# Kernel optimization log

Measured on AMD Instinct MI355X. Metric: run time of the kernel, lower is better.

Reference implementation:

```python
import jax, jax.numpy as jnp
import numpy as np

GRID_SIZE = 5


def kan_layer(x, spline_weight, spline_scaler, grid):
    # x: (B, In); spline_weight: (Out, In, G); spline_scaler: (Out, In); grid: (G,)
    xn = jnp.tanh(x)                                   # (B, In)
    # distances: (B, Out, In, G) via broadcast of (B,1,In,1) against (G,)
    distances = jnp.abs(xn[:, None, :, None] - grid)
    weights = jnp.exp(-distances * spline_scaler[None, :, :, None])
    # double sum over grid then in_features, fused into one einsum
    return jnp.einsum('boig,oig->bo', weights, spline_weight)


def setup_inputs() -> dict:
    key = jax.random.key(0)
    ks = jax.random.split(key, 7)
    B, D_IN, D_H, D_OUT = 2048, 128, 256, 64
    return {
        'x':  jax.random.normal(ks[0], (B, D_IN), dtype=jnp.float32),
        'w1': jax.random.normal(ks[1], (D_H, D_IN, GRID_SIZE), dtype=jnp.float32),
        's1': jax.random.normal(ks[2], (D_H, D_IN), dtype=jnp.float32),
        'w2': jax.random.normal(ks[3], (D_H // 2, D_H, GRID_SIZE), dtype=jnp.float32),
        's2': jax.random.normal(ks[4], (D_H // 2, D_H), dtype=jnp.float32),
        'w3': jax.random.normal(ks[5], (D_OUT, D_H // 2, GRID_SIZE), dtype=jnp.float32),
        's3': jax.random.normal(ks[6], (D_OUT, D_H // 2), dtype=jnp.float32),
    }


def reference(x, w1, s1, w2, s2, w3, s3):
    grid = jnp.linspace(-1.0, 1.0, GRID_SIZE, dtype=jnp.float32)  # registered buffer
    h1 = jax.nn.relu(kan_layer(x, w1, s1, grid))
    h2 = jax.nn.relu(kan_layer(h1, w2, s2, grid))
    out = jax.nn.sigmoid(kan_layer(h2, w3, s3, grid))
    return out
```

## Files before the change

kernel.cpp:

```cpp
#include <hip/hip_runtime.h>
#include <math.h>

#define GRID_N 5
#define LOG2E 1.4426950408889634f
#define EXP2F __builtin_amdgcn_exp2f

__device__ __forceinline__ void prep_one(const float* __restrict__ w,
                                         const float* __restrict__ s,
                                         float* __restrict__ T, float* __restrict__ Kt,
                                         int O, int I, int idx) {
    int o = idx / I, i = idx % I;
    float K = -s[idx] * LOG2E;
    const float gv[5] = {-1.f, -0.5f, 0.f, 0.5f, 1.f};
    float A[6], B[6];
    A[0] = 0.f; B[5] = 0.f;
#pragma unroll
    for (int g = 0; g < 5; g++)
        A[g + 1] = A[g] + w[idx * GRID_N + g] * EXP2F(-K * gv[g]);
#pragma unroll
    for (int g = 4; g >= 0; g--)
        B[g] = B[g + 1] + w[idx * GRID_N + g] * EXP2F(K * gv[g]);
#pragma unroll
    for (int k = 0; k < 6; k++) {
        T[((i * 6 + k) * O + o) * 2 + 0] = A[k];
        T[((i * 6 + k) * O + o) * 2 + 1] = B[k];
    }
    Kt[i * O + o] = K;
}

__global__ __launch_bounds__(256) void prep_all(
    const float* __restrict__ w1, const float* __restrict__ s1, float* T1, float* K1,
    const float* __restrict__ w2, const float* __restrict__ s2, float* T2, float* K2,
    const float* __restrict__ w3, const float* __restrict__ s3, float* T3, float* K3) {
    int idx = blockIdx.x * 256 + threadIdx.x;
    if (idx < 32768)       prep_one(w1, s1, T1, K1, 256, 128, idx);
    else if (idx < 65536)  prep_one(w2, s2, T2, K2, 128, 256, idx - 32768);
    else if (idx < 73728)  prep_one(w3, s3, T3, K3,  64, 128, idx - 65536);
}

template<int IN, int OUT, int ACT, int BPT>
__global__ __launch_bounds__(256, 4) void kan_layer(
    const float* __restrict__ xin,
    const char*  __restrict__ Tb,
    const float* __restrict__ Kt,
    float* __restrict__ out)
{
    constexpr int CH  = IN / 64;
    constexpr int NBG = 2048 / BPT;
    constexpr unsigned ROWB = OUT * 8;

    const int lane = threadIdx.x & 63;
    const int wid  = (blockIdx.x << 2) | (threadIdx.x >> 6);
    const int oc   = wid / NBG;
    const int bg   = wid % NBG;
    const int o    = (oc << 6) | lane;
    const int b0   = bg * BPT;

    float    xv[BPT][CH];
    unsigned off[BPT][CH];
#pragma unroll
    for (int j = 0; j < BPT; j++)
#pragma unroll
        for (int c = 0; c < CH; c++) {
            int   i  = (c << 6) + lane;
            float v  = xin[(b0 + j) * IN + i];
            float ex = EXP2F(2.0f * LOG2E * v);
            float t  = 1.0f - 2.0f / (ex + 1.0f);
            xv[j][c] = t;
            int k = (int)((t + 1.0f) * 2.0f) + 1;
            k = k > 5 ? 5 : k;
            off[j][c] = (unsigned)(i * 6 + k) * ROWB;
        }

    float acc[BPT];
#pragma unroll
    for (int j = 0; j < BPT; j++) acc[j] = 0.f;

    const unsigned o8 = (unsigned)o * 8u;
    const float*   Kp = Kt + o;

#pragma unroll
    for (int c = 0; c < CH; c++) {
        for (int lb = 0; lb < 8; lb++) {
            float2 ab[BPT][8];
            float  Kv[8];
#pragma unroll
            for (int u = 0; u < 8; u++) {
                const int l = lb * 8 + u;
                const int i = (c << 6) + l;
                Kv[u] = Kp[i * OUT];
#pragma unroll
                for (int j = 0; j < BPT; j++) {
                    unsigned os = (unsigned)__builtin_amdgcn_readlane((int)off[j][c], l);
                    ab[j][u] = *(const float2*)(Tb + (os + o8));
                }
            }
#pragma unroll
            for (int u = 0; u < 8; u++) {
                const int l = lb * 8 + u;
#pragma unroll
                for (int j = 0; j < BPT; j++) {
                    float xs = __int_as_float(__builtin_amdgcn_readlane(__float_as_int(xv[j][c]), l));
                    float t  = Kv[u] * xs;
                    acc[j] += ab[j][u].x * EXP2F(t) + ab[j][u].y * EXP2F(-t);
                }
            }
        }
    }

#pragma unroll
    for (int j = 0; j < BPT; j++) {
        float z = acc[j];
        if (ACT == 0) z = fmaxf(z, 0.f);
        else          z = 1.0f / (1.0f + EXP2F(-LOG2E * z));
        out[(b0 + j) * OUT + o] = z;
    }
}

extern "C" void kernel_launch(void* const* d_in, const int* in_sizes, int n_in,
                              void* d_out, int out_size, void* d_ws, size_t ws_size,
                              hipStream_t stream) {
    const float* x  = (const float*)d_in[0];
    const float* w1 = (const float*)d_in[1];
    const float* s1 = (const float*)d_in[2];
    const float* w2 = (const float*)d_in[3];
    const float* s2 = (const float*)d_in[4];
    const float* w3 = (const float*)d_in[5];
    const float* s3 = (const float*)d_in[6];
    float* out = (float*)d_out;

    float* ws  = (float*)d_ws;
    float* h1  = ws;
    float* h2  = h1  + 524288;
    float* T1  = h2  + 262144;
    float* K1  = T1  + 393216;
    float* T2  = K1  + 32768;
    float* K2  = T2  + 393216;
    float* T3  = K2  + 32768;
    float* K3  = T3  + 98304;

    prep_all<<<288, 256, 0, stream>>>(w1, s1, T1, K1, w2, s2, T2, K2, w3, s3, T3, K3);

    kan_layer<128, 256, 0, 2><<<1024, 256, 0, stream>>>(x,  (const char*)T1, K1, h1);
    kan_layer<256, 128, 0, 2><<< 512, 256, 0, stream>>>(h1, (const char*)T2, K2, h2);
    kan_layer<128,  64, 1, 1><<< 512, 256, 0, stream>>>(h2, (const char*)T3, K3, out);
}
```

Measured before the change: 96.77 us.

## Split input dimension across waves with partial sums and one batch row per wave

Each wave now handles a single batch row instead of two, and layers 2 and 3 split the input-feature reduction into two halves. The halves write partial sums that the next stage adds together: layer 3 sums them and applies ReLU on load, and a new small kernel sums layer 3's partials and applies the sigmoid. Launch bounds rise to 8 blocks per CU and grid sizes grow, aiming for more waves in flight and less register pressure. The cost is an extra kernel launch, a larger partial-sum buffer, and losing the table-load and readlane reuse that two rows per wave gave.

```diff
diff --git a/kernel.cpp b/kernel.cpp
--- a/kernel.cpp
+++ b/kernel.cpp
@@ -4,6 +4,7 @@
 #define GRID_N 5
 #define LOG2E 1.4426950408889634f
 #define EXP2F __builtin_amdgcn_exp2f
+#define BATCH 2048
 
 __device__ __forceinline__ void prep_one(const float* __restrict__ w,
                                          const float* __restrict__ s,
@@ -38,83 +39,88 @@
     else if (idx < 73728)  prep_one(w3, s3, T3, K3,  64, 128, idx - 65536);
 }
 
-template<int IN, int OUT, int ACT, int BPT>
-__global__ __launch_bounds__(256, 4) void kan_layer(
+template<int IN, int OUT, int ACT, int ISPLIT, int XMODE>
+__global__ __launch_bounds__(256, 8) void kan_layer(
     const float* __restrict__ xin,
     const char*  __restrict__ Tb,
     const float* __restrict__ Kt,
-    float* __restrict__ out)
+    float* __restrict__ outp)
 {
-    constexpr int CH  = IN / 64;
-    constexpr int NBG = 2048 / BPT;
+    constexpr int LEN = IN / ISPLIT;
+    constexpr int CH  = LEN / 64;
     constexpr unsigned ROWB = OUT * 8;
 
     const int lane = threadIdx.x & 63;
     const int wid  = (blockIdx.x << 2) | (threadIdx.x >> 6);
-    const int oc   = wid / NBG;
-    const int bg   = wid % NBG;
+    const int oc   = wid / (BATCH * ISPLIT);
+    const int rem  = wid % (BATCH * ISPLIT);
+    const int half = rem / BATCH;
+    const int b    = rem % BATCH;
     const int o    = (oc << 6) | lane;
-    const int b0   = bg * BPT;
+    const int ibase = half * LEN;
 
-    float    xv[BPT][CH];
-    unsigned off[BPT][CH];
+    float    xv[CH];
+    unsigned off[CH];
 #pragma unroll
-    for (int j = 0; j < BPT; j++)
-#pragma unroll
-        for (int c = 0; c < CH; c++) {
-            int   i  = (c << 6) + lane;
-            float v  = xin[(b0 + j) * IN + i];
-            float ex = EXP2F(2.0f * LOG2E * v);
-            float t  = 1.0f - 2.0f / (ex + 1.0f);
-            xv[j][c] = t;
-            int k = (int)((t + 1.0f) * 2.0f) + 1;
-            k = k > 5 ? 5 : k;
-            off[j][c] = (unsigned)(i * 6 + k) * ROWB;
+    for (int c = 0; c < CH; c++) {
+        int   i = ibase + (c << 6) + lane;
+        float v;
+        if (XMODE == 0) {
+            v = xin[b * IN + i];
+        } else {
+            v = fmaxf(xin[b * IN + i] + xin[(BATCH * IN) + b * IN + i], 0.f);
         }
+        float ex = EXP2F(2.0f * LOG2E * v);
+        float t  = 1.0f - 2.0f / (ex + 1.0f);
+        xv[c] = t;
+        int k = (int)((t + 1.0f) * 2.0f) + 1;
+        k = k > 5 ? 5 : k;
+        off[c] = (unsigned)(i * 6 + k) * ROWB;
+    }
 
-    float acc[BPT];
-#pragma unroll
-    for (int j = 0; j < BPT; j++) acc[j] = 0.f;
-
+    float acc = 0.f;
     const unsigned o8 = (unsigned)o * 8u;
     const float*   Kp = Kt + o;
 
 #pragma unroll
     for (int c = 0; c < CH; c++) {
         for (int lb = 0; lb < 8; lb++) {
-            float2 ab[BPT][8];
+            float2 ab[8];
             float  Kv[8];
 #pragma unroll
             for (int u = 0; u < 8; u++) {
                 const int l = lb * 8 + u;
-                const int i = (c << 6) + l;
+                const int i = ibase + (c << 6) + l;
                 Kv[u] = Kp[i * OUT];
-#pragma unroll
-                for (int j = 0; j < BPT; j++) {
-                    unsigned os = (unsigned)__builtin_amdgcn_readlane((int)off[j][c], l);
-                    ab[j][u] = *(const float2*)(Tb + (os + o8));
-                }
+                unsigned os = (unsigned)__builtin_amdgcn_readlane((int)off[c], l);
+                ab[u] = *(const float2*)(Tb + (os + o8));
             }
 #pragma unroll
             for (int u = 0; u < 8; u++) {
                 const int l = lb * 8 + u;
-#pragma unroll
-                for (int j = 0; j < BPT; j++) {
-                    float xs = __int_as_float(__builtin_amdgcn_readlane(__float_as_int(xv[j][c]), l));
-                    float t  = Kv[u] * xs;
-                    acc[j] += ab[j][u].x * EXP2F(t) + ab[j][u].y * EXP2F(-t);
-                }
+                float xs = __int_as_float(__builtin_amdgcn_readlane(__float_as_int(xv[c]), l));
+                float t  = Kv[u] * xs;
+                acc += ab[u].x * EXP2F(t) + ab[u].y * EXP2F(-t);
             }
         }
     }
 
-#pragma unroll
-    for (int j = 0; j < BPT; j++) {
-        float z = acc[j];
+    if (ISPLIT == 1) {
+        float z = acc;
         if (ACT == 0) z = fmaxf(z, 0.f);
         else          z = 1.0f / (1.0f + EXP2F(-LOG2E * z));
-        out[(b0 + j) * OUT + o] = z;
+        outp[b * OUT + o] = z;
+    } else {
+        outp[(half * BATCH + b) * OUT + o] = acc;
     }
+}
+
+__global__ __launch_bounds__(256) void sigmoid_combine(
+    const float* __restrict__ p, float* __restrict__ out, int n) {
+    int e = blockIdx.x * 256 + threadIdx.x;
+    if (e >= n) return;
+    float z = p[e] + p[n + e];
+    out[e] = 1.0f / (1.0f + EXP2F(-LOG2E * z));
 }
 
 extern "C" void kernel_launch(void* const* d_in, const int* in_sizes, int n_in,
@@ -131,17 +137,19 @@
 
     float* ws  = (float*)d_ws;
     float* h1  = ws;
-    float* h2  = h1  + 524288;
-    float* T1  = h2  + 262144;
+    float* p2  = h1  + 524288;
+    float* T1  = p2  + 524288;
     float* K1  = T1  + 393216;
     float* T2  = K1  + 32768;
     float* K2  = T2  + 393216;
     float* T3  = K2  + 32768;
     float* K3  = T3  + 98304;
+    float* p3  = h1;
 
     prep_all<<<288, 256, 0, stream>>>(w1, s1, T1, K1, w2, s2, T2, K2, w3, s3, T3, K3);
 
-    kan_layer<128, 256, 0, 2><<<1024, 256, 0, stream>>>(x,  (const char*)T1, K1, h1);
-    kan_layer<256, 128, 0, 2><<< 512, 256, 0, stream>>>(h1, (const char*)T2, K2, h2);
-    kan_layer<128,  64, 1, 1><<< 512, 256, 0, stream>>>(h2, (const char*)T3, K3, out);
+    kan_layer<128, 256, 0, 1, 0><<<2048, 256, 0, stream>>>(x,  (const char*)T1, K1, h1);
+    kan_layer<256, 128, 0, 2, 0><<<2048, 256, 0, stream>>>(h1, (const char*)T2, K2, p2);
+    kan_layer<128,  64, 1, 2, 1><<<1024, 256, 0, stream>>>(p2, (const char*)T3, K3, p3);
+    sigmoid_combine<<<512, 256, 0, stream>>>(p3, out, 131072);
 }
```

After: 106.4 us. 10.0% more time.

## Restructure KAN layers with transposed activations, interleaved per-edge records, and split-K partial sums

Applied to the files above, without the earlier changes.

Activations are transposed to input-major so each lane owns a batch element and reads are coalesced. Spline tables are repacked into one 48-byte record per (input, output) pair, holding the prefix sums and the scaler, which removes the separate K array and the readlane broadcasts. The input dimension is split across blocks, with partial sums written out and combined in small kernels that also apply relu+tanh or sigmoid. This adds several kernel launches and extra global round trips for the partial sums. Each lane also does per-lane gathers at different segment offsets within its record.

```diff
diff --git a/kernel.cpp b/kernel.cpp
--- a/kernel.cpp
+++ b/kernel.cpp
@@ -4,117 +4,133 @@
 #define GRID_N 5
 #define LOG2E 1.4426950408889634f
 #define EXP2F __builtin_amdgcn_exp2f
+#define B 2048
+
+__device__ __forceinline__ float tanh_fast(float v) {
+    float e = EXP2F(2.0f * LOG2E * v);
+    return 1.0f - 2.0f / (e + 1.0f);
+}
 
 __device__ __forceinline__ void prep_one(const float* __restrict__ w,
                                          const float* __restrict__ s,
-                                         float* __restrict__ T, float* __restrict__ Kt,
-                                         int O, int I, int idx) {
+                                         float* __restrict__ T, int O, int I, int idx) {
     int o = idx / I, i = idx % I;
     float K = -s[idx] * LOG2E;
     const float gv[5] = {-1.f, -0.5f, 0.f, 0.5f, 1.f};
-    float A[6], B[6];
-    A[0] = 0.f; B[5] = 0.f;
+    float A[6], Bb[6];
+    A[0] = 0.f; Bb[5] = 0.f;
 #pragma unroll
     for (int g = 0; g < 5; g++)
         A[g + 1] = A[g] + w[idx * GRID_N + g] * EXP2F(-K * gv[g]);
 #pragma unroll
     for (int g = 4; g >= 0; g--)
-        B[g] = B[g + 1] + w[idx * GRID_N + g] * EXP2F(K * gv[g]);
+        Bb[g] = Bb[g + 1] + w[idx * GRID_N + g] * EXP2F(K * gv[g]);
+    float* r = T + ((size_t)i * O + o) * 12;
 #pragma unroll
-    for (int k = 0; k < 6; k++) {
-        T[((i * 6 + k) * O + o) * 2 + 0] = A[k];
-        T[((i * 6 + k) * O + o) * 2 + 1] = B[k];
+    for (int k = 1; k <= 5; k++) {
+        r[2 * (k - 1)]     = A[k];
+        r[2 * (k - 1) + 1] = Bb[k];
     }
-    Kt[i * O + o] = K;
+    r[10] = K;
+    r[11] = 0.f;
 }
 
-__global__ __launch_bounds__(256) void prep_all(
-    const float* __restrict__ w1, const float* __restrict__ s1, float* T1, float* K1,
-    const float* __restrict__ w2, const float* __restrict__ s2, float* T2, float* K2,
-    const float* __restrict__ w3, const float* __restrict__ s3, float* T3, float* K3) {
+__global__ __launch_bounds__(256) void prep_tables(
+    const float* __restrict__ w1, const float* __restrict__ s1, float* T1,
+    const float* __restrict__ w2, const float* __restrict__ s2, float* T2,
+    const float* __restrict__ w3, const float* __restrict__ s3, float* T3) {
     int idx = blockIdx.x * 256 + threadIdx.x;
-    if (idx < 32768)       prep_one(w1, s1, T1, K1, 256, 128, idx);
-    else if (idx < 65536)  prep_one(w2, s2, T2, K2, 128, 256, idx - 32768);
-    else if (idx < 73728)  prep_one(w3, s3, T3, K3,  64, 128, idx - 65536);
+    if (idx < 32768)       prep_one(w1, s1, T1, 256, 128, idx);
+    else if (idx < 65536)  prep_one(w2, s2, T2, 128, 256, idx - 32768);
+    else if (idx < 73728)  prep_one(w3, s3, T3,  64, 128, idx - 65536);
 }
 
-template<int IN, int OUT, int ACT, int BPT>
-__global__ __launch_bounds__(256, 4) void kan_layer(
-    const float* __restrict__ xin,
+__global__ __launch_bounds__(256) void transpose_tanh(
+    const float* __restrict__ x, float* __restrict__ xT) {
+    __shared__ float lds[64][65];
+    const int tx = threadIdx.x & 63, ty = threadIdx.x >> 6;
+    const int b0 = (blockIdx.x & 31) << 6, i0 = (blockIdx.x >> 5) << 6;
+#pragma unroll
+    for (int rr = 0; rr < 16; rr++) {
+        int r = rr * 4 + ty;
+        lds[r][tx] = tanh_fast(x[(size_t)(b0 + r) * 128 + i0 + tx]);
+    }
+    __syncthreads();
+#pragma unroll
+    for (int rr = 0; rr < 16; rr++) {
+        int r = rr * 4 + ty;
+        xT[(size_t)(i0 + r) * B + b0 + tx] = lds[tx][r];
+    }
+}
+
+template<int LEN, int OUT, int NSPLIT>
+__global__ __launch_bounds__(256) void kan_g(
+    const float* __restrict__ xnT,
     const char*  __restrict__ Tb,
-    const float* __restrict__ Kt,
-    float* __restrict__ out)
+    float* __restrict__ outp)
 {
-    constexpr int CH  = IN / 64;
-    constexpr int NBG = 2048 / BPT;
-    constexpr unsigned ROWB = OUT * 8;
+    constexpr int NOG = OUT / 4;
+    const int lane = threadIdx.x & 63;
+    const int widx = __builtin_amdgcn_readfirstlane(threadIdx.x >> 6);
+    const int bq   = blockIdx.x & 7;
+    const int og   = (blockIdx.x >> 3) % NOG;
+    const int h    = (blockIdx.x >> 3) / NOG;
+    const int bg   = bq * 4 + widx;
+    const int gb   = (bg << 6) + lane;
+    const int ibase = h * LEN;
+    const int oabs  = og * 4;
 
-    const int lane = threadIdx.x & 63;
-    const int wid  = (blockIdx.x << 2) | (threadIdx.x >> 6);
-    const int oc   = wid / NBG;
-    const int bg   = wid % NBG;
-    const int o    = (oc << 6) | lane;
-    const int b0   = bg * BPT;
+    float acc[4] = {0.f, 0.f, 0.f, 0.f};
 
-    float    xv[BPT][CH];
-    unsigned off[BPT][CH];
+#pragma unroll 1
+    for (int c = 0; c < LEN / 8; c++) {
+        const int ic = ibase + c * 8;
+        float xs[8];
+        int   koff[8];
 #pragma unroll
-    for (int j = 0; j < BPT; j++)
+        for (int u = 0; u < 8; u++)
+            xs[u] = xnT[(size_t)(ic + u) * B + gb];
 #pragma unroll
-        for (int c = 0; c < CH; c++) {
-            int   i  = (c << 6) + lane;
-            float v  = xin[(b0 + j) * IN + i];
-            float ex = EXP2F(2.0f * LOG2E * v);
-            float t  = 1.0f - 2.0f / (ex + 1.0f);
-            xv[j][c] = t;
-            int k = (int)((t + 1.0f) * 2.0f) + 1;
-            k = k > 5 ? 5 : k;
-            off[j][c] = (unsigned)(i * 6 + k) * ROWB;
+        for (int u = 0; u < 8; u++) {
+            int k = (int)(xs[u] * 2.0f + 2.0f);
+            koff[u] = (k > 4 ? 4 : k) << 3;
         }
-
-    float acc[BPT];
 #pragma unroll
-    for (int j = 0; j < BPT; j++) acc[j] = 0.f;
-
-    const unsigned o8 = (unsigned)o * 8u;
-    const float*   Kp = Kt + o;
-
+        for (int u = 0; u < 8; u++) {
+            const char* rec = Tb + ((size_t)(ic + u) * OUT + oabs) * 48;
 #pragma unroll
-    for (int c = 0; c < CH; c++) {
-        for (int lb = 0; lb < 8; lb++) {
-            float2 ab[BPT][8];
-            float  Kv[8];
-#pragma unroll
-            for (int u = 0; u < 8; u++) {
-                const int l = lb * 8 + u;
-                const int i = (c << 6) + l;
-                Kv[u] = Kp[i * OUT];
-#pragma unroll
-                for (int j = 0; j < BPT; j++) {
-                    unsigned os = (unsigned)__builtin_amdgcn_readlane((int)off[j][c], l);
-                    ab[j][u] = *(const float2*)(Tb + (os + o8));
-                }
-            }
-#pragma unroll
-            for (int u = 0; u < 8; u++) {
-                const int l = lb * 8 + u;
-#pragma unroll
-                for (int j = 0; j < BPT; j++) {
-                    float xs = __int_as_float(__builtin_amdgcn_readlane(__float_as_int(xv[j][c]), l));
-                    float t  = Kv[u] * xs;
-                    acc[j] += ab[j][u].x * EXP2F(t) + ab[j][u].y * EXP2F(-t);
-                }
+            for (int o = 0; o < 4; o++) {
+                float2 ab = *(const float2*)(rec + o * 48 + koff[u]);
+                float  Kv = *(const float*)(rec + o * 48 + 40);
+                float  t  = Kv * xs[u];
+                acc[o] += ab.x * EXP2F(t) + ab.y * EXP2F(-t);
             }
         }
     }
 
 #pragma unroll
-    for (int j = 0; j < BPT; j++) {
-        float z = acc[j];
-        if (ACT == 0) z = fmaxf(z, 0.f);
-        else          z = 1.0f / (1.0f + EXP2F(-LOG2E * z));
-        out[(b0 + j) * OUT + o] = z;
-    }
+    for (int o = 0; o < 4; o++)
+        outp[((size_t)h * OUT + oabs + o) * B + gb] = acc[o];
+}
+
+template<int NP>
+__global__ __launch_bounds__(256) void combine_tanh(
+    const float* __restrict__ p, float* __restrict__ out, int n) {
+    int e = blockIdx.x * 256 + threadIdx.x;
+    if (e >= n) return;
+    float z = p[e];
+#pragma unroll
+    for (int q = 1; q < NP; q++) z += p[(size_t)q * n + e];
+    out[e] = tanh_fast(fmaxf(z, 0.f));
+}
+
+__global__ __launch_bounds__(256) void sigmoid_combine_t(
+    const float* __restrict__ p, float* __restrict__ out, int n) {
+    int e = blockIdx.x * 256 + threadIdx.x;
+    if (e >= n) return;
+    float z = p[e] + p[n + e] + p[2 * n + e] + p[3 * n + e];
+    int b = e & (B - 1), o = e >> 11;
+    out[b * 64 + o] = 1.0f / (1.0f + EXP2F(-LOG2E * z));
 }
 
 extern "C" void kernel_launch(void* const* d_in, const int* in_sizes, int n_in,
@@ -130,18 +146,20 @@
     float* out = (float*)d_out;
 
     float* ws  = (float*)d_ws;
-    float* h1  = ws;
-    float* h2  = h1  + 524288;
-    float* T1  = h2  + 262144;
-    float* K1  = T1  + 393216;
-    float* T2  = K1  + 32768;
-    float* K2  = T2  + 393216;
-    float* T3  = K2  + 32768;
-    float* K3  = T3  + 98304;
+    float* U   = ws;
+    float* V   = U + 1048576;
+    float* W   = V + 262144;
+    float* T1  = W + 524288;
+    float* T2  = T1 + 393216;
+    float* T3  = T2 + 393216;
 
-    prep_all<<<288, 256, 0, stream>>>(w1, s1, T1, K1, w2, s2, T2, K2, w3, s3, T3, K3);
+    transpose_tanh<<<64, 256, 0, stream>>>(x, V);
+    prep_tables<<<288, 256, 0, stream>>>(w1, s1, T1, w2, s2, T2, w3, s3, T3);
 
-    kan_layer<128, 256, 0, 2><<<1024, 256, 0, stream>>>(x,  (const char*)T1, K1, h1);
-    kan_layer<256, 128, 0, 2><<< 512, 256, 0, stream>>>(h1, (const char*)T2, K2, h2);
-    kan_layer<128,  64, 1, 1><<< 512, 256, 0, stream>>>(h2, (const char*)T3, K3, out);
+    kan_g<64, 256, 2><<<1024, 256, 0, stream>>>(V, (const char*)T1, U);
+    combine_tanh<2><<<2048, 256, 0, stream>>>(U, W, 524288);
+    kan_g<64, 128, 4><<<1024, 256, 0, stream>>>(W, (const char*)T2, U);
+    combine_tanh<4><<<1024, 256, 0, stream>>>(U, V, 262144);
+    kan_g<32, 64, 4><<<512, 256, 0, stream>>>(V, (const char*)T3, W);
+    sigmoid_combine_t<<<512, 256, 0, stream>>>(W, out, 131072);
 }
```

Result: slower. 107.1 us (+10.7%).
